# Optimization experiments

Measured on AMD Instinct MI355X. Metric: run time of the kernel, lower is better.

## Reference

```python
import jax, jax.numpy as jnp
import numpy as np
from jax import lax

VOCAB, H, B, T = 2514, 300, 128, 512

def setup_inputs() -> dict:
    key = jax.random.key(0)
    ks = jax.random.split(key, 12)
    s = 1.0 / np.sqrt(H)
    inp = {
        'x': jax.random.randint(ks[0], (B, T), 0, VOCAB),
        'emb': jax.random.normal(ks[1], (VOCAB, H), jnp.float32),
        'Wih0': jax.random.uniform(ks[2], (4 * H, H), jnp.float32, -s, s),
        'Whh0': jax.random.uniform(ks[3], (4 * H, H), jnp.float32, -s, s),
        'bih0': jax.random.uniform(ks[4], (4 * H,), jnp.float32, -s, s),
        'bhh0': jax.random.uniform(ks[5], (4 * H,), jnp.float32, -s, s),
        'Wih1': jax.random.uniform(ks[6], (4 * H, H), jnp.float32, -s, s),
        'Whh1': jax.random.uniform(ks[7], (4 * H, H), jnp.float32, -s, s),
        'bih1': jax.random.uniform(ks[8], (4 * H,), jnp.float32, -s, s),
        'bhh1': jax.random.uniform(ks[9], (4 * H,), jnp.float32, -s, s),
        'Wout': jax.random.uniform(ks[10], (VOCAB, H), jnp.float32, -s, s),
        'bout': jax.random.uniform(ks[11], (VOCAB,), jnp.float32, -s, s),
    }
    return inp


def lstm_layer(x, Wih, Whh, bih, bhh):
    # x: [B, T, H] -> [B, T, H]. PyTorch gate order: i, f, g, o.
    b, t, _ = x.shape
    h = Whh.shape[1]
    xg = jnp.einsum('bti,gi->btg', x, Wih) + (bih + bhh)  # [B, T, 4H]
    h0 = jnp.zeros((b, h), x.dtype)
    c0 = jnp.zeros((b, h), x.dtype)

    def step(carry, g_t):
        hp, cp = carry
        gates = g_t + hp @ Whh.T
        i, f, g, o = jnp.split(gates, 4, axis=-1)
        c = jax.nn.sigmoid(f) * cp + jax.nn.sigmoid(i) * jnp.tanh(g)
        hh = jax.nn.sigmoid(o) * jnp.tanh(c)
        return (hh, c), hh

    _, ys = lax.scan(step, (h0, c0), jnp.swapaxes(xg, 0, 1))  # [T, B, H]
    return jnp.swapaxes(ys, 0, 1)


def reference(x, emb, Wih0, Whh0, bih0, bhh0, Wih1, Whh1, bih1, bhh1, Wout, bout):
    e = emb[x]                                   # [B, T, H]
    h1 = lstm_layer(e, Wih0, Whh0, bih0, bhh0)   # layer 1
    h2 = lstm_layer(h1, Wih1, Whh1, bih1, bhh1)  # layer 2
    logits = jnp.einsum('bth,vh->btv', h2, Wout) + bout
    return logits.reshape(-1, logits.shape[-1])  # [B*T, VOCAB]
```

## Files before the change

kernel.cpp:

```cpp
#include <hip/hip_runtime.h>
#include <cstdint>
#include <cstddef>

namespace {

constexpr int H    = 300;
constexpr int G4   = 1200;
constexpr int B    = 128;
constexpr int T    = 512;
constexpr int NVOC = 2514;

typedef __attribute__((ext_vector_type(8))) short  short8;
typedef __attribute__((ext_vector_type(4))) float  f32x4;

__device__ __forceinline__ float sigm(float x)     { return 1.f / (1.f + __expf(-x)); }
__device__ __forceinline__ float tanhfast(float x) { return 1.f - 2.f / (__expf(2.f*x) + 1.f); }

__device__ __forceinline__ unsigned short bf16_rn(float f) {
    unsigned u = __float_as_uint(f);
    u += 0x7FFFu + ((u >> 16) & 1u);
    return (unsigned short)(u >> 16);
}
__device__ __forceinline__ float bf16_f(unsigned short s) {
    return __uint_as_float(((unsigned)s) << 16);
}
__device__ __forceinline__ unsigned pack2(unsigned short lo16, unsigned short hi16) {
    return (unsigned)lo16 | ((unsigned)hi16 << 16);
}

constexpr int TSEG = 15 * 128 * 20;

template<int AMODE, bool HASB2>
__global__ __launch_bounds__(256)
void gemm_mfma(const float* __restrict__ A, const float* __restrict__ W,
               const float* __restrict__ b1, const float* __restrict__ b2,
               const int* __restrict__ tok, float* __restrict__ out, int N)
{
    __shared__ __align__(16) unsigned short Ah[128][40], Al[128][40];
    __shared__ __align__(16) unsigned short Wh[128][40], Wl[128][40];

    const int tid = threadIdx.x;
    const int m0 = blockIdx.y * 128, n0 = blockIdx.x * 128;
    const int rl = tid >> 1, cb = (tid & 1) * 16;

    const int m = m0 + rl;
    const float* aptr;
    if (AMODE == 0) aptr = A + (size_t)m * H;
    else if (AMODE == 3) aptr = A + (size_t)(m & 511) * TSEG + (m >> 9) * 20;
    else {
        const int q = ((m & 127) << 9) + (m >> 7);
        aptr = A + (size_t)((AMODE == 1) ? tok[q] : q) * H;
    }
    const int nrow = n0 + rl;
    const float* wptr = W + (size_t)nrow * H;
    const bool nok = (nrow < N);

    const int wv = tid >> 6, lane = tid & 63;
    const int mw = (wv >> 1) * 64, nw = (wv & 1) * 64;
    const int kg = lane >> 4, mm = lane & 15;

    f32x4 acc[4][4];
#pragma unroll
    for (int i = 0; i < 4; ++i)
#pragma unroll
        for (int j = 0; j < 4; ++j) acc[i][j] = (f32x4){0.f, 0.f, 0.f, 0.f};

    for (int kt = 0; kt < 10; ++kt) {
        const int kbase = kt * 32;
        float4 av[4], wvv[4];
#pragma unroll
        for (int j = 0; j < 4; ++j) {
            const int col = kbase + cb + j * 4;
            const bool kv = (col <= H - 4);
            if (AMODE == 3)
                av[j] = kv ? *(const float4*)(aptr + (col / 20) * 2560 + col % 20)
                           : make_float4(0, 0, 0, 0);
            else
                av[j] = kv ? *(const float4*)(aptr + col) : make_float4(0, 0, 0, 0);
            wvv[j] = (kv && nok) ? *(const float4*)(wptr + col) : make_float4(0, 0, 0, 0);
        }
        __syncthreads();
#pragma unroll
        for (int j = 0; j < 4; ++j) {
            const float a[4] = {av[j].x,  av[j].y,  av[j].z,  av[j].w};
            const float w[4] = {wvv[j].x, wvv[j].y, wvv[j].z, wvv[j].w};
            unsigned short ah[4], al_[4], wh[4], wl[4];
#pragma unroll
            for (int e = 0; e < 4; ++e) {
                ah[e] = bf16_rn(a[e]); al_[e] = bf16_rn(a[e] - bf16_f(ah[e]));
                wh[e] = bf16_rn(w[e]); wl[e]  = bf16_rn(w[e] - bf16_f(wh[e]));
            }
            const int cc = cb + j * 4;
            *(uint2*)&Ah[rl][cc] = make_uint2(pack2(ah[0],ah[1]),  pack2(ah[2],ah[3]));
            *(uint2*)&Al[rl][cc] = make_uint2(pack2(al_[0],al_[1]),pack2(al_[2],al_[3]));
            *(uint2*)&Wh[rl][cc] = make_uint2(pack2(wh[0],wh[1]),  pack2(wh[2],wh[3]));
            *(uint2*)&Wl[rl][cc] = make_uint2(pack2(wl[0],wl[1]),  pack2(wl[2],wl[3]));
        }
        __syncthreads();

        short8 fah[4], fal[4], fbh[4], fbl[4];
#pragma unroll
        for (int f = 0; f < 4; ++f) {
            fah[f] = *(const short8*)&Ah[mw + f*16 + mm][kg*8];
            fal[f] = *(const short8*)&Al[mw + f*16 + mm][kg*8];
            fbh[f] = *(const short8*)&Wh[nw + f*16 + mm][kg*8];
            fbl[f] = *(const short8*)&Wl[nw + f*16 + mm][kg*8];
        }
#pragma unroll
        for (int mf = 0; mf < 4; ++mf)
#pragma unroll
            for (int nf = 0; nf < 4; ++nf) {
                acc[mf][nf] = __builtin_amdgcn_mfma_f32_16x16x32_bf16(fah[mf], fbh[nf], acc[mf][nf], 0, 0, 0);
                acc[mf][nf] = __builtin_amdgcn_mfma_f32_16x16x32_bf16(fal[mf], fbh[nf], acc[mf][nf], 0, 0, 0);
                acc[mf][nf] = __builtin_amdgcn_mfma_f32_16x16x32_bf16(fah[mf], fbl[nf], acc[mf][nf], 0, 0, 0);
            }
    }

    float bias[4];
#pragma unroll
    for (int nf = 0; nf < 4; ++nf) {
        const int n = n0 + nw + nf*16 + mm;
        float v = 0.f;
        if (n < N) { v = b1[n]; if (HASB2) v += b2[n]; }
        bias[nf] = v;
    }
    const int qr = lane >> 4;
#pragma unroll
    for (int mf = 0; mf < 4; ++mf) {
        const int row = m0 + mw + mf*16 + qr*4;
        float* orow = out + (size_t)row * N;
#pragma unroll
        for (int nf = 0; nf < 4; ++nf) {
            const int n = n0 + nw + nf*16 + mm;
            if (n < N) {
#pragma unroll
                for (int r = 0; r < 4; ++r)
                    orow[(size_t)r * N + n] = acc[mf][nf][r] + bias[nf];
            }
        }
    }
}

constexpr unsigned SENT = 0x7FB00F0Fu;

__global__ __launch_bounds__(256)
void sentinel_fill(uint4* __restrict__ p, size_t n4)
{
    const uint4 s = make_uint4(SENT, SENT, SENT, SENT);
    size_t i = (size_t)blockIdx.x * blockDim.x + threadIdx.x;
    const size_t stride = (size_t)gridDim.x * blockDim.x;
    for (; i < n4; i += stride) p[i] = s;
}

constexpr int HGC = 15;
constexpr int BGC = 16;
constexpr int NWG = HGC * BGC;
constexpr int A2OFF = 20480;
constexpr int APARF = 40960;
constexpr int GDOFF = 2 * APARF;
constexpr int FLDS  = GDOFF + 10 * 8 * 16 * 4;

struct StageCtx {
    size_t   src64[5];
    int      aoffHi[5];
    unsigned pend0;
};

__device__ __forceinline__ void stage_init(StageCtx& S, int lane, int bg,
                                           int base_hg, int nchunks, int region)
{
    const int words = nchunks * 80;
    S.pend0 = 0;
#pragma unroll
    for (int j = 0; j < 5; ++j) {
        const int s = lane + 64 * j;
        const bool ok = (s < words);
        const int chunk = ok ? s / 80 : 0, rem = ok ? s % 80 : 0;
        const int hg = base_hg + chunk;
        S.src64[j] = (size_t)(hg * 128 + bg * 8) * 10 + rem;
        const int u2 = rem * 2, b_loc = u2 / 20, u = u2 % 20;
        const int k = hg * 20 + u;
        const int kt = k >> 5, kq = (k >> 3) & 3, pos = k & 7;
        S.aoffHi[j] = region + ((kt * 2) * 4 + kq) * 256 + b_loc * 16 + pos * 2;
        if (ok) S.pend0 |= 1u << j;
    }
}

__device__ __forceinline__ void stage_poll(const StageCtx& S,
                                           const float* __restrict__ slice,
                                           unsigned char* Ap)
{
    const unsigned long long* s64 = (const unsigned long long*)slice;
    unsigned long long val[5];
    unsigned pend = S.pend0;
    while (__any(pend != 0)) {
        unsigned long long w[5];
#pragma unroll
        for (int j = 0; j < 5; ++j)
            if (pend & (1u << j))
                w[j] = __hip_atomic_load(s64 + S.src64[j], __ATOMIC_RELAXED,
                                         __HIP_MEMORY_SCOPE_AGENT);
#pragma unroll
        for (int j = 0; j < 5; ++j)
            if (pend & (1u << j)) {
                const unsigned long long x = w[j];
                if ((unsigned)x != SENT && (unsigned)(x >> 32) != SENT) {
                    val[j] = x; pend &= ~(1u << j);
                }
            }
    }
#pragma unroll
    for (int j = 0; j < 5; ++j)
        if (S.pend0 & (1u << j)) {
            const float v0 = __uint_as_float((unsigned)val[j]);
            const float v1 = __uint_as_float((unsigned)(val[j] >> 32));
            const unsigned short h0 = bf16_rn(v0), h1_ = bf16_rn(v1);
            *(unsigned*)(Ap + S.aoffHi[j]) = pack2(h0, h1_);
            *(unsigned*)(Ap + S.aoffHi[j] + 1024) =
                pack2(bf16_rn(v0 - bf16_f(h0)), bf16_rn(v1 - bf16_f(h1_)));
        }
}

template<int NTN>
__device__ void fused_g0(int lane, int hg, int bg, int NT0, int base_hg,
                         int nchunks,
                         const float* __restrict__ xg0,
                         const float* __restrict__ Whh0,
                         float* __restrict__ h1p,
                         unsigned char* __restrict__ Abuf, float (*gd)[8][16])
{
    const int kg = lane >> 4, mm = lane & 15;

    short8 bh[10][NTN], bl[10][NTN];
#pragma unroll
    for (int kt = 0; kt < 10; ++kt)
#pragma unroll
        for (int j = 0; j < NTN; ++j) {
            const int c = (NT0 + j) * 16 + mm;
            const int grow = (c & 3) * H + hg * 20 + (c >> 2);
            short8 hi, lo;
#pragma unroll
            for (int e = 0; e < 8; ++e) {
                const int k = kt * 32 + kg * 8 + e;
                const float v = (k < H) ? Whh0[(size_t)grow * H + k] : 0.f;
                const unsigned short h16 = bf16_rn(v);
                hi[e] = (short)h16;
                lo[e] = (short)bf16_rn(v - bf16_f(h16));
            }
            bh[kt][j] = hi; bl[kt][j] = lo;
        }

    StageCtx S; stage_init(S, lane, bg, base_hg, nchunks, 0);

    const int sh = (NTN == 2) ? 3 : 2;
    const bool upd = lane < (NTN << 5);
    const int b_u = lane >> sh, u4 = lane & ((1 << sh) - 1);
    const int u_loc = NT0 * 4 + u4;
    const int ntl = NT0 + (u4 >> 2), u_rel = u4 & 3;
    float cst = 0.f;

    const float* xb0 = xg0 + (size_t)(bg * 8 + b_u) * G4 + hg * 20 + u_loc;
    float* hst = h1p + ((size_t)hg * 128 + bg * 8 + b_u) * 20 + u_loc;

    for (int it = 0; it <= T; ++it) {
        float xv0 = 0.f, xv1 = 0.f, xv2 = 0.f, xv3 = 0.f;
        if (upd && it < T) {
            const float* xb = xb0 + (size_t)it * B * G4;
            xv0 = xb[0]; xv1 = xb[H]; xv2 = xb[2 * H]; xv3 = xb[3 * H];
        }
        unsigned char* Ap = Abuf + (it & 1) * APARF;
        if (it >= 1) stage_poll(S, h1p + (size_t)(it - 1) * TSEG, Ap);
        __syncthreads();

        if (it < T) {
            f32x4 a0 = (f32x4){0.f,0.f,0.f,0.f}, a1 = (f32x4){0.f,0.f,0.f,0.f};
#pragma unroll
            for (int kt = 0; kt < 10; ++kt) {
                const short8 ah = *(const short8*)(Ap + ((kt*2+0)*4 + kg)*256 + mm*16);
                const short8 al = *(const short8*)(Ap + ((kt*2+1)*4 + kg)*256 + mm*16);
                a0 = __builtin_amdgcn_mfma_f32_16x16x32_bf16(ah, bh[kt][0], a0, 0, 0, 0);
                a0 = __builtin_amdgcn_mfma_f32_16x16x32_bf16(al, bh[kt][0], a0, 0, 0, 0);
                a0 = __builtin_amdgcn_mfma_f32_16x16x32_bf16(ah, bl[kt][0], a0, 0, 0, 0);
                if (NTN > 1) {
                    a1 = __builtin_amdgcn_mfma_f32_16x16x32_bf16(ah, bh[kt][1], a1, 0, 0, 0);
                    a1 = __builtin_amdgcn_mfma_f32_16x16x32_bf16(al, bh[kt][1], a1, 0, 0, 0);
                    a1 = __builtin_amdgcn_mfma_f32_16x16x32_bf16(ah, bl[kt][1], a1, 0, 0, 0);
                }
            }
            if (lane < 32) {
                const int br = (lane >> 4) * 4;
#pragma unroll
                for (int r = 0; r < 4; ++r) gd[NT0][br + r][mm] = a0[r];
                if (NTN > 1)
#pragma unroll
                    for (int r = 0; r < 4; ++r) gd[NT0 + 1][br + r][mm] = a1[r];
            }
            if (upd) {
                const float* g4 = &gd[ntl][b_u][u_rel * 4];
                const float gi = xv0 + g4[0], gf = xv1 + g4[1];
                const float gz = xv2 + g4[2], go = xv3 + g4[3];
                const float iG = sigm(gi), fG = sigm(gf);
                const float zG = tanhfast(gz), oG = sigm(go);
                cst = fmaf(fG, cst, iG * zG);
                const float hv = oG * tanhfast(cst);
                __hip_atomic_store(hst + (size_t)it * TSEG, hv,
                                   __ATOMIC_RELAXED, __HIP_MEMORY_SCOPE_AGENT);
            }
        }
    }
}

__device__ void fused_g1(int lane, int hg, int bg, int ntg,
                         const float* __restrict__ stage_src, int stage_delta,
                         int stage_region, int base_hg, int nchunks,
                         const float* __restrict__ Wih1,
                         const float* __restrict__ Whh1,
                         const float* __restrict__ bih1,
                         const float* __restrict__ bhh1,
                         float* __restrict__ h2p,
                         unsigned char* __restrict__ Abuf, float (*gd)[8][16])
{
    const int kg = lane >> 4, mm = lane & 15;
    const int c = ntg * 16 + mm;
    const int grow = (c & 3) * H + hg * 20 + (c >> 2);

    short8 bIh[10], bIl[10], bHh[10], bHl[10];
#pragma unroll
    for (int kt = 0; kt < 10; ++kt) {
        short8 ih, il, hh, hl;
#pragma unroll
        for (int e = 0; e < 8; ++e) {
            const int k = kt * 32 + kg * 8 + e;
            const float vi = (k < H) ? Wih1[(size_t)grow * H + k] : 0.f;
            const float vh = (k < H) ? Whh1[(size_t)grow * H + k] : 0.f;
            const unsigned short i16 = bf16_rn(vi), h16 = bf16_rn(vh);
            ih[e] = (short)i16; il[e] = (short)bf16_rn(vi - bf16_f(i16));
            hh[e] = (short)h16; hl[e] = (short)bf16_rn(vh - bf16_f(h16));
        }
        bIh[kt] = ih; bIl[kt] = il; bHh[kt] = hh; bHl[kt] = hl;
    }

    StageCtx S; stage_init(S, lane, bg, base_hg, nchunks, stage_region);

    const bool upd = lane < 32;
    const int b_u = lane >> 2, u4 = lane & 3;
    const int u_loc = ntg * 4 + u4;
    float bias[4];
#pragma unroll
    for (int g = 0; g < 4; ++g) {
        const int gr = g * H + hg * 20 + u_loc;
        bias[g] = bih1[gr] + bhh1[gr];
    }
    float cst = 0.f;
    float* hst = h2p + ((size_t)hg * 128 + bg * 8 + b_u) * 20 + u_loc;

    for (int it = 0; it <= T; ++it) {
        unsigned char* Ap = Abuf + (it & 1) * APARF;
        if (it >= stage_delta)
            stage_poll(S, stage_src + (size_t)(it - stage_delta) * TSEG, Ap);
        __syncthreads();

        if (it >= 1) {
            f32x4 acc = (f32x4){0.f, 0.f, 0.f, 0.f};
#pragma unroll
            for (int kt = 0; kt < 10; ++kt) {
                const short8 ah = *(const short8*)(Ap + ((kt*2+0)*4 + kg)*256 + mm*16);
                const short8 al = *(const short8*)(Ap + ((kt*2+1)*4 + kg)*256 + mm*16);
                acc = __builtin_amdgcn_mfma_f32_16x16x32_bf16(ah, bIh[kt], acc, 0, 0, 0);
                acc = __builtin_amdgcn_mfma_f32_16x16x32_bf16(al, bIh[kt], acc, 0, 0, 0);
                acc = __builtin_amdgcn_mfma_f32_16x16x32_bf16(ah, bIl[kt], acc, 0, 0, 0);
            }
#pragma unroll
            for (int kt = 0; kt < 10; ++kt) {
                const short8 ah = *(const short8*)(Ap + A2OFF + ((kt*2+0)*4 + kg)*256 + mm*16);
                const short8 al = *(const short8*)(Ap + A2OFF + ((kt*2+1)*4 + kg)*256 + mm*16);
                acc = __builtin_amdgcn_mfma_f32_16x16x32_bf16(ah, bHh[kt], acc, 0, 0, 0);
                acc = __builtin_amdgcn_mfma_f32_16x16x32_bf16(al, bHh[kt], acc, 0, 0, 0);
                acc = __builtin_amdgcn_mfma_f32_16x16x32_bf16(ah, bHl[kt], acc, 0, 0, 0);
            }
            if (lane < 32) {
                const int br = (lane >> 4) * 4;
#pragma unroll
                for (int r = 0; r < 4; ++r) gd[5 + ntg][br + r][mm] = acc[r];
            }
            if (upd) {
                const float* g4 = &gd[5 + ntg][b_u][u4 * 4];
                const float gi = bias[0] + g4[0], gf = bias[1] + g4[1];
                const float gz = bias[2] + g4[2], go = bias[3] + g4[3];
                const float iG = sigm(gi), fG = sigm(gf);
                const float zG = tanhfast(gz), oG = sigm(go);
                cst = fmaf(fG, cst, iG * zG);
                const float hv = oG * tanhfast(cst);
                __hip_atomic_store(hst + (size_t)(it - 1) * TSEG, hv,
                                   __ATOMIC_RELAXED, __HIP_MEMORY_SCOPE_AGENT);
            }
        }
    }
}

__global__ __launch_bounds__(512, 2)
void lstm_fused(const float* __restrict__ xg0,
                const float* __restrict__ Whh0,
                const float* __restrict__ Wih1,
                const float* __restrict__ Whh1,
                const float* __restrict__ bih1,
                const float* __restrict__ bhh1,
                float* __restrict__ h1p, float* __restrict__ h2p)
{
    extern __shared__ unsigned char smem[];
    unsigned char* Abuf = smem;
    float (*gd)[8][16] = (float(*)[8][16])(smem + GDOFF);

    const int tid = threadIdx.x, wv = tid >> 6, lane = tid & 63;
    const int hg = blockIdx.x % HGC, bg = blockIdx.x / HGC;

    for (int i = tid; i < FLDS / 16; i += 512)
        ((uint4*)smem)[i] = make_uint4(0, 0, 0, 0);
    __syncthreads();

    if      (wv == 0) fused_g0<2>(lane, hg, bg, 0,  0, 4, xg0, Whh0, h1p, Abuf, gd);
    else if (wv == 1) fused_g0<2>(lane, hg, bg, 2,  4, 4, xg0, Whh0, h1p, Abuf, gd);
    else if (wv == 2) fused_g0<1>(lane, hg, bg, 4,  8, 4, xg0, Whh0, h1p, Abuf, gd);
    else if (wv == 3) fused_g1(lane, hg, bg, 0, h1p, 1, 0,     12, 3,
                               Wih1, Whh1, bih1, bhh1, h2p, Abuf, gd);
    else              fused_g1(lane, hg, bg, wv - 3, h2p, 2, A2OFF,
                               (wv - 4) * 4, (wv == 7) ? 3 : 4,
                               Wih1, Whh1, bih1, bhh1, h2p, Abuf, gd);
}

}

extern "C" void kernel_launch(void* const* d_in, const int* in_sizes, int n_in,
                              void* d_out, int out_size, void* d_ws, size_t ws_size,
                              hipStream_t stream)
{
    const int*   x    = (const int*)  d_in[0];
    const float* emb  = (const float*)d_in[1];
    const float* Wih0 = (const float*)d_in[2];
    const float* Whh0 = (const float*)d_in[3];
    const float* bih0 = (const float*)d_in[4];
    const float* bhh0 = (const float*)d_in[5];
    const float* Wih1 = (const float*)d_in[6];
    const float* Whh1 = (const float*)d_in[7];
    const float* bih1 = (const float*)d_in[8];
    const float* bhh1 = (const float*)d_in[9];
    const float* Wout = (const float*)d_in[10];
    const float* bout = (const float*)d_in[11];

    float* out = (float*)d_out;
    float* xg = (float*)d_out;
    float* h1p = (float*)d_ws;
    float* h2p = h1p + (size_t)B * T * H;

    const size_t nh = 2 * (size_t)B * T * H;
    sentinel_fill<<<dim3(2048), dim3(256), 0, stream>>>((uint4*)h1p, nh / 4);

    hipFuncSetAttribute(reinterpret_cast<const void*>(lstm_fused),
                        hipFuncAttributeMaxDynamicSharedMemorySize, FLDS);

    const dim3 blk(256);
    gemm_mfma<1, true ><<<dim3(10, 512), blk, 0, stream>>>(emb, Wih0, bih0, bhh0, x, xg, G4);
    lstm_fused<<<dim3(NWG), dim3(512), FLDS, stream>>>(xg, Whh0, Wih1, Whh1,
                                                       bih1, bhh1, h1p, h2p);
    gemm_mfma<3, false><<<dim3(20, 512), blk, 0, stream>>>(h2p, Wout, bout, nullptr, nullptr, out, NVOC);
}
```

Before: 3.675 ms.

## Fuse layer-0 input projection into persistent LSTM kernel with packed bf16 hi/lo hidden states

The separate embedding-gather GEMM for layer 0's input gates is removed. Each step's embedding rows are now staged into LDS, and Wih0 is multiplied inside the persistent LSTM kernel alongside Whh0. The embedding and output weights are pre-converted once into packed bf16 hi/lo words, and hidden states are stored packed, so no float-to-bf16 split is needed when staging or in the final GEMM. The recurrent weights now use only the hi part for Whh, which is a reduced-precision 2-term product. The work is also redistributed across waves: five layer-0 waves and three layer-1 waves. This adds MFMA work per step inside the serial recurrence and uses more LDS.

Measured after the change: 3.159 ms. 14.0% less time.

```diff
diff --git a/kernel.cpp b/kernel.cpp
--- a/kernel.cpp
+++ b/kernel.cpp
@@ -9,6 +9,7 @@
 constexpr int B    = 128;
 constexpr int T    = 512;
 constexpr int NVOC = 2514;
+constexpr int KP   = 304;
 
 typedef __attribute__((ext_vector_type(8))) short  short8;
 typedef __attribute__((ext_vector_type(4))) float  f32x4;
@@ -27,14 +28,39 @@
 __device__ __forceinline__ unsigned pack2(unsigned short lo16, unsigned short hi16) {
     return (unsigned)lo16 | ((unsigned)hi16 << 16);
 }
+__device__ __forceinline__ unsigned pack_hl(float v) {
+    const unsigned short hi = bf16_rn(v);
+    const unsigned short lo = bf16_rn(v - bf16_f(hi));
+    return (unsigned)hi | ((unsigned)lo << 16);
+}
 
 constexpr int TSEG = 15 * 128 * 20;
 
-template<int AMODE, bool HASB2>
+constexpr unsigned SENTP = 0x7FB07FB0u;
+
 __global__ __launch_bounds__(256)
-void gemm_mfma(const float* __restrict__ A, const float* __restrict__ W,
-               const float* __restrict__ b1, const float* __restrict__ b2,
-               const int* __restrict__ tok, float* __restrict__ out, int N)
+void sentinel_fill(uint4* __restrict__ p, size_t n4)
+{
+    const uint4 s = make_uint4(SENTP, SENTP, SENTP, SENTP);
+    size_t i = (size_t)blockIdx.x * blockDim.x + threadIdx.x;
+    const size_t stride = (size_t)gridDim.x * blockDim.x;
+    for (; i < n4; i += stride) p[i] = s;
+}
+
+__global__ __launch_bounds__(256)
+void preconv(const float* __restrict__ src, unsigned* __restrict__ dst, int rows)
+{
+    const size_t n = (size_t)rows * KP;
+    for (size_t i = (size_t)blockIdx.x * 256 + threadIdx.x; i < n;
+         i += (size_t)gridDim.x * 256) {
+        const int c = (int)(i % KP), r = (int)(i / KP);
+        dst[i] = (c < H) ? pack_hl(src[(size_t)r * H + c]) : 0u;
+    }
+}
+
+__global__ __launch_bounds__(256)
+void gemm_pk(const unsigned* __restrict__ Apk, const unsigned* __restrict__ Wpk,
+             const float* __restrict__ b1, float* __restrict__ out, int N)
 {
     __shared__ __align__(16) unsigned short Ah[128][40], Al[128][40];
     __shared__ __align__(16) unsigned short Wh[128][40], Wl[128][40];
@@ -44,15 +70,9 @@
     const int rl = tid >> 1, cb = (tid & 1) * 16;
 
     const int m = m0 + rl;
-    const float* aptr;
-    if (AMODE == 0) aptr = A + (size_t)m * H;
-    else if (AMODE == 3) aptr = A + (size_t)(m & 511) * TSEG + (m >> 9) * 20;
-    else {
-        const int q = ((m & 127) << 9) + (m >> 7);
-        aptr = A + (size_t)((AMODE == 1) ? tok[q] : q) * H;
-    }
+    const unsigned* aptr = Apk + (size_t)(m & 511) * TSEG + (m >> 9) * 20;
     const int nrow = n0 + rl;
-    const float* wptr = W + (size_t)nrow * H;
+    const unsigned* wptr = Wpk + (size_t)nrow * KP;
     const bool nok = (nrow < N);
 
     const int wv = tid >> 6, lane = tid & 63;
@@ -66,35 +86,28 @@
         for (int j = 0; j < 4; ++j) acc[i][j] = (f32x4){0.f, 0.f, 0.f, 0.f};
 
     for (int kt = 0; kt < 10; ++kt) {
-        const int kbase = kt * 32;
-        float4 av[4], wvv[4];
+        uint4 pa[4], pw[4];
 #pragma unroll
         for (int j = 0; j < 4; ++j) {
-            const int col = kbase + cb + j * 4;
-            const bool kv = (col <= H - 4);
-            if (AMODE == 3)
-                av[j] = kv ? *(const float4*)(aptr + (col / 20) * 2560 + col % 20)
-                           : make_float4(0, 0, 0, 0);
-            else
-                av[j] = kv ? *(const float4*)(aptr + col) : make_float4(0, 0, 0, 0);
-            wvv[j] = (kv && nok) ? *(const float4*)(wptr + col) : make_float4(0, 0, 0, 0);
+            const int col = kt * 32 + cb + j * 4;
+            pa[j] = (col < 300)
+                  ? *(const uint4*)(aptr + (col / 20) * 2560 + col % 20)
+                  : make_uint4(0, 0, 0, 0);
+            pw[j] = (nok && col < KP) ? *(const uint4*)(wptr + col)
+                                      : make_uint4(0, 0, 0, 0);
         }
         __syncthreads();
 #pragma unroll
         for (int j = 0; j < 4; ++j) {
-            const float a[4] = {av[j].x,  av[j].y,  av[j].z,  av[j].w};
-            const float w[4] = {wvv[j].x, wvv[j].y, wvv[j].z, wvv[j].w};
-            unsigned short ah[4], al_[4], wh[4], wl[4];
-#pragma unroll
-            for (int e = 0; e < 4; ++e) {
-                ah[e] = bf16_rn(a[e]); al_[e] = bf16_rn(a[e] - bf16_f(ah[e]));
-                wh[e] = bf16_rn(w[e]); wl[e]  = bf16_rn(w[e] - bf16_f(wh[e]));
-            }
             const int cc = cb + j * 4;
-            *(uint2*)&Ah[rl][cc] = make_uint2(pack2(ah[0],ah[1]),  pack2(ah[2],ah[3]));
-            *(uint2*)&Al[rl][cc] = make_uint2(pack2(al_[0],al_[1]),pack2(al_[2],al_[3]));
-            *(uint2*)&Wh[rl][cc] = make_uint2(pack2(wh[0],wh[1]),  pack2(wh[2],wh[3]));
-            *(uint2*)&Wl[rl][cc] = make_uint2(pack2(wl[0],wl[1]),  pack2(wl[2],wl[3]));
+            *(uint2*)&Ah[rl][cc] = make_uint2((pa[j].x & 0xFFFFu) | (pa[j].y << 16),
+                                              (pa[j].z & 0xFFFFu) | (pa[j].w << 16));
+            *(uint2*)&Al[rl][cc] = make_uint2((pa[j].x >> 16) | (pa[j].y & 0xFFFF0000u),
+                                              (pa[j].z >> 16) | (pa[j].w & 0xFFFF0000u));
+            *(uint2*)&Wh[rl][cc] = make_uint2((pw[j].x & 0xFFFFu) | (pw[j].y << 16),
+                                              (pw[j].z & 0xFFFFu) | (pw[j].w << 16));
+            *(uint2*)&Wl[rl][cc] = make_uint2((pw[j].x >> 16) | (pw[j].y & 0xFFFF0000u),
+                                              (pw[j].z >> 16) | (pw[j].w & 0xFFFF0000u));
         }
         __syncthreads();
 
@@ -120,9 +133,7 @@
 #pragma unroll
     for (int nf = 0; nf < 4; ++nf) {
         const int n = n0 + nw + nf*16 + mm;
-        float v = 0.f;
-        if (n < N) { v = b1[n]; if (HASB2) v += b2[n]; }
-        bias[nf] = v;
+        bias[nf] = (n < N) ? b1[n] : 0.f;
     }
     const int qr = lane >> 4;
 #pragma unroll
@@ -141,24 +152,15 @@
     }
 }
 
-constexpr unsigned SENT = 0x7FB00F0Fu;
-
-__global__ __launch_bounds__(256)
-void sentinel_fill(uint4* __restrict__ p, size_t n4)
-{
-    const uint4 s = make_uint4(SENT, SENT, SENT, SENT);
-    size_t i = (size_t)blockIdx.x * blockDim.x + threadIdx.x;
-    const size_t stride = (size_t)gridDim.x * blockDim.x;
-    for (; i < n4; i += stride) p[i] = s;
-}
-
 constexpr int HGC = 15;
 constexpr int BGC = 16;
 constexpr int NWG = HGC * BGC;
-constexpr int A2OFF = 20480;
-constexpr int APARF = 40960;
-constexpr int GDOFF = 2 * APARF;
-constexpr int FLDS  = GDOFF + 10 * 8 * 16 * 4;
+constexpr int A2OFF  = 20480;
+constexpr int EOFF   = 40960;
+constexpr int APARF  = 61440;
+constexpr int GDOFF  = 2 * APARF;
+constexpr int TOKOFF = GDOFF + 10*8*16*4;
+constexpr int FLDS   = TOKOFF + 8*512*4;
 
 struct StageCtx {
     size_t   src64[5];
@@ -180,14 +182,14 @@
         S.src64[j] = (size_t)(hg * 128 + bg * 8) * 10 + rem;
         const int u2 = rem * 2, b_loc = u2 / 20, u = u2 % 20;
         const int k = hg * 20 + u;
-        const int kt = k >> 5, kq = (k >> 3) & 3, pos = k & 7;
-        S.aoffHi[j] = region + ((kt * 2) * 4 + kq) * 256 + b_loc * 16 + pos * 2;
+        S.aoffHi[j] = region + ((k >> 5) * 8 + ((k >> 3) & 3)) * 256
+                    + b_loc * 16 + (k & 7) * 2;
         if (ok) S.pend0 |= 1u << j;
     }
 }
 
 __device__ __forceinline__ void stage_poll(const StageCtx& S,
-                                           const float* __restrict__ slice,
+                                           const unsigned* __restrict__ slice,
                                            unsigned char* Ap)
 {
     const unsigned long long* s64 = (const unsigned long long*)slice;
@@ -204,7 +206,7 @@
         for (int j = 0; j < 5; ++j)
             if (pend & (1u << j)) {
                 const unsigned long long x = w[j];
-                if ((unsigned)x != SENT && (unsigned)(x >> 32) != SENT) {
+                if ((unsigned)x != SENTP && (unsigned)(x >> 32) != SENTP) {
                     val[j] = x; pend &= ~(1u << j);
                 }
             }
@@ -212,176 +214,209 @@
 #pragma unroll
     for (int j = 0; j < 5; ++j)
         if (S.pend0 & (1u << j)) {
-            const float v0 = __uint_as_float((unsigned)val[j]);
-            const float v1 = __uint_as_float((unsigned)(val[j] >> 32));
-            const unsigned short h0 = bf16_rn(v0), h1_ = bf16_rn(v1);
-            *(unsigned*)(Ap + S.aoffHi[j]) = pack2(h0, h1_);
-            *(unsigned*)(Ap + S.aoffHi[j] + 1024) =
-                pack2(bf16_rn(v0 - bf16_f(h0)), bf16_rn(v1 - bf16_f(h1_)));
-        }
-}
-
-template<int NTN>
-__device__ void fused_g0(int lane, int hg, int bg, int NT0, int base_hg,
-                         int nchunks,
-                         const float* __restrict__ xg0,
+            const unsigned p0 = (unsigned)val[j], p1 = (unsigned)(val[j] >> 32);
+            *(unsigned*)(Ap + S.aoffHi[j])        = (p0 & 0xFFFFu) | (p1 << 16);
+            *(unsigned*)(Ap + S.aoffHi[j] + 1024) = (p0 >> 16) | (p1 & 0xFFFF0000u);
+        }
+}
+
+struct ECtx { int b[3]; int koff[3]; int aoff[3]; bool ok[3]; };
+
+__device__ __forceinline__ void estage_init(ECtx& E, int tid)
+{
+#pragma unroll
+    for (int j = 0; j < 3; ++j) {
+        const int es = tid + 512 * j;
+        E.ok[j] = (es < 1216);
+        const int bb = E.ok[j] ? es / 152 : 0;
+        const int kp = E.ok[j] ? es % 152 : 0;
+        const int k  = kp * 2;
+        E.b[j]    = bb;
+        E.koff[j] = k;
+        E.aoff[j] = EOFF + ((k >> 5) * 8 + ((k >> 3) & 3)) * 256
+                  + bb * 16 + (k & 7) * 2;
+    }
+}
+
+__device__ __forceinline__ void estage(const ECtx& E, const int* __restrict__ tokL,
+                                       const unsigned* __restrict__ embcv, int it,
+                                       unsigned char* Ap)
+{
+#pragma unroll
+    for (int j = 0; j < 3; ++j)
+        if (E.ok[j]) {
+            const int tok = tokL[E.b[j] * 512 + it];
+            const unsigned long long w = *(const unsigned long long*)
+                (embcv + (size_t)tok * KP + E.koff[j]);
+            const unsigned p0 = (unsigned)w, p1 = (unsigned)(w >> 32);
+            *(unsigned*)(Ap + E.aoff[j])        = (p0 & 0xFFFFu) | (p1 << 16);
+            *(unsigned*)(Ap + E.aoff[j] + 1024) = (p0 >> 16) | (p1 & 0xFFFF0000u);
+        }
+}
+
+__device__ void fused_L0(int lane, int nt, int hg, int bg,
+                         const unsigned* __restrict__ embcv,
+                         const float* __restrict__ Wih0,
                          const float* __restrict__ Whh0,
-                         float* __restrict__ h1p,
+                         const float* __restrict__ bih0,
+                         const float* __restrict__ bhh0,
+                         unsigned* __restrict__ h1p,
+                         const unsigned* __restrict__ ssrc, int sreg, int sbase,
+                         int snch, int sdel,
+                         const ECtx& E, const int* __restrict__ tokL,
                          unsigned char* __restrict__ Abuf, float (*gd)[8][16])
 {
     const int kg = lane >> 4, mm = lane & 15;
 
-    short8 bh[10][NTN], bl[10][NTN];
-#pragma unroll
-    for (int kt = 0; kt < 10; ++kt)
-#pragma unroll
-        for (int j = 0; j < NTN; ++j) {
-            const int c = (NT0 + j) * 16 + mm;
-            const int grow = (c & 3) * H + hg * 20 + (c >> 2);
-            short8 hi, lo;
-#pragma unroll
-            for (int e = 0; e < 8; ++e) {
-                const int k = kt * 32 + kg * 8 + e;
-                const float v = (k < H) ? Whh0[(size_t)grow * H + k] : 0.f;
-                const unsigned short h16 = bf16_rn(v);
-                hi[e] = (short)h16;
-                lo[e] = (short)bf16_rn(v - bf16_f(h16));
-            }
-            bh[kt][j] = hi; bl[kt][j] = lo;
-        }
-
-    StageCtx S; stage_init(S, lane, bg, base_hg, nchunks, 0);
-
-    const int sh = (NTN == 2) ? 3 : 2;
-    const bool upd = lane < (NTN << 5);
-    const int b_u = lane >> sh, u4 = lane & ((1 << sh) - 1);
-    const int u_loc = NT0 * 4 + u4;
-    const int ntl = NT0 + (u4 >> 2), u_rel = u4 & 3;
+    short8 bhh[10], bih[10], bil[10];
+#pragma unroll
+    for (int kt = 0; kt < 10; ++kt) {
+        const int c = nt * 16 + mm;
+        const int grow = (c & 3) * H + hg * 20 + (c >> 2);
+        short8 h_, ih_, il_;
+#pragma unroll
+        for (int e = 0; e < 8; ++e) {
+            const int k = kt * 32 + kg * 8 + e;
+            const float vh = (k < H) ? Whh0[(size_t)grow * H + k] : 0.f;
+            const float vi = (k < H) ? Wih0[(size_t)grow * H + k] : 0.f;
+            h_[e] = (short)bf16_rn(vh);
+            const unsigned short i16 = bf16_rn(vi);
+            ih_[e] = (short)i16;
+            il_[e] = (short)bf16_rn(vi - bf16_f(i16));
+        }
+        bhh[kt] = h_; bih[kt] = ih_; bil[kt] = il_;
+    }
+
+    StageCtx S; stage_init(S, lane, bg, sbase, snch, sreg);
+
+    const bool upd = lane < 32;
+    const int b_u = lane >> 2, u4 = lane & 3;
+    const int u_loc = nt * 4 + u4;
+    float bias[4];
+#pragma unroll
+    for (int g = 0; g < 4; ++g)
+        bias[g] = bih0[g * H + hg * 20 + u_loc] + bhh0[g * H + hg * 20 + u_loc];
     float cst = 0.f;
-
-    const float* xb0 = xg0 + (size_t)(bg * 8 + b_u) * G4 + hg * 20 + u_loc;
-    float* hst = h1p + ((size_t)hg * 128 + bg * 8 + b_u) * 20 + u_loc;
+    unsigned* hst = h1p + ((size_t)hg * 128 + bg * 8 + b_u) * 20 + u_loc;
 
     for (int it = 0; it <= T; ++it) {
-        float xv0 = 0.f, xv1 = 0.f, xv2 = 0.f, xv3 = 0.f;
-        if (upd && it < T) {
-            const float* xb = xb0 + (size_t)it * B * G4;
-            xv0 = xb[0]; xv1 = xb[H]; xv2 = xb[2 * H]; xv3 = xb[3 * H];
-        }
         unsigned char* Ap = Abuf + (it & 1) * APARF;
-        if (it >= 1) stage_poll(S, h1p + (size_t)(it - 1) * TSEG, Ap);
+        if (it < T) estage(E, tokL, embcv, it, Ap);
+        if (it >= sdel) stage_poll(S, ssrc + (size_t)(it - sdel) * TSEG, Ap);
         __syncthreads();
 
         if (it < T) {
-            f32x4 a0 = (f32x4){0.f,0.f,0.f,0.f}, a1 = (f32x4){0.f,0.f,0.f,0.f};
+            f32x4 acc = (f32x4){0.f, 0.f, 0.f, 0.f};
 #pragma unroll
             for (int kt = 0; kt < 10; ++kt) {
-                const short8 ah = *(const short8*)(Ap + ((kt*2+0)*4 + kg)*256 + mm*16);
-                const short8 al = *(const short8*)(Ap + ((kt*2+1)*4 + kg)*256 + mm*16);
-                a0 = __builtin_amdgcn_mfma_f32_16x16x32_bf16(ah, bh[kt][0], a0, 0, 0, 0);
-                a0 = __builtin_amdgcn_mfma_f32_16x16x32_bf16(al, bh[kt][0], a0, 0, 0, 0);
-                a0 = __builtin_amdgcn_mfma_f32_16x16x32_bf16(ah, bl[kt][0], a0, 0, 0, 0);
-                if (NTN > 1) {
-                    a1 = __builtin_amdgcn_mfma_f32_16x16x32_bf16(ah, bh[kt][1], a1, 0, 0, 0);
-                    a1 = __builtin_amdgcn_mfma_f32_16x16x32_bf16(al, bh[kt][1], a1, 0, 0, 0);
-                    a1 = __builtin_amdgcn_mfma_f32_16x16x32_bf16(ah, bl[kt][1], a1, 0, 0, 0);
-                }
+                const int boff = (kt * 8 + kg) * 256 + mm * 16;
+                const short8 eh = *(const short8*)(Ap + EOFF + boff);
+                const short8 el = *(const short8*)(Ap + EOFF + boff + 1024);
+                const short8 hh = *(const short8*)(Ap + boff);
+                const short8 hl = *(const short8*)(Ap + boff + 1024);
+                acc = __builtin_amdgcn_mfma_f32_16x16x32_bf16(eh, bih[kt], acc, 0, 0, 0);
+                acc = __builtin_amdgcn_mfma_f32_16x16x32_bf16(el, bih[kt], acc, 0, 0, 0);
+                acc = __builtin_amdgcn_mfma_f32_16x16x32_bf16(eh, bil[kt], acc, 0, 0, 0);
+                acc = __builtin_amdgcn_mfma_f32_16x16x32_bf16(hh, bhh[kt], acc, 0, 0, 0);
+                acc = __builtin_amdgcn_mfma_f32_16x16x32_bf16(hl, bhh[kt], acc, 0, 0, 0);
             }
             if (lane < 32) {
                 const int br = (lane >> 4) * 4;
 #pragma unroll
-                for (int r = 0; r < 4; ++r) gd[NT0][br + r][mm] = a0[r];
-                if (NTN > 1)
-#pragma unroll
-                    for (int r = 0; r < 4; ++r) gd[NT0 + 1][br + r][mm] = a1[r];
+                for (int r = 0; r < 4; ++r) gd[nt][br + r][mm] = acc[r];
             }
             if (upd) {
-                const float* g4 = &gd[ntl][b_u][u_rel * 4];
-                const float gi = xv0 + g4[0], gf = xv1 + g4[1];
-                const float gz = xv2 + g4[2], go = xv3 + g4[3];
+                const float* g4 = &gd[nt][b_u][u4 * 4];
+                const float gi = bias[0] + g4[0], gf = bias[1] + g4[1];
+                const float gz = bias[2] + g4[2], go = bias[3] + g4[3];
                 const float iG = sigm(gi), fG = sigm(gf);
                 const float zG = tanhfast(gz), oG = sigm(go);
                 cst = fmaf(fG, cst, iG * zG);
                 const float hv = oG * tanhfast(cst);
-                __hip_atomic_store(hst + (size_t)it * TSEG, hv,
+                __hip_atomic_store(hst + (size_t)it * TSEG, pack_hl(hv),
                                    __ATOMIC_RELAXED, __HIP_MEMORY_SCOPE_AGENT);
             }
         }
     }
 }
 
-__device__ void fused_g1(int lane, int hg, int bg, int ntg,
-                         const float* __restrict__ stage_src, int stage_delta,
-                         int stage_region, int base_hg, int nchunks,
+template<int NTL>
+__device__ void fused_L1(int lane, int t0, int hg, int bg,
+                         const unsigned* __restrict__ embcv,
                          const float* __restrict__ Wih1,
                          const float* __restrict__ Whh1,
                          const float* __restrict__ bih1,
                          const float* __restrict__ bhh1,
-                         float* __restrict__ h2p,
+                         unsigned* __restrict__ h2p,
+                         const unsigned* __restrict__ ssrc, int sreg, int sbase,
+                         int snch, int sdel,
+                         const ECtx& E, const int* __restrict__ tokL,
                          unsigned char* __restrict__ Abuf, float (*gd)[8][16])
 {
     const int kg = lane >> 4, mm = lane & 15;
-    const int c = ntg * 16 + mm;
-    const int grow = (c & 3) * H + hg * 20 + (c >> 2);
-
-    short8 bIh[10], bIl[10], bHh[10], bHl[10];
-#pragma unroll
-    for (int kt = 0; kt < 10; ++kt) {
-        short8 ih, il, hh, hl;
-#pragma unroll
-        for (int e = 0; e < 8; ++e) {
-            const int k = kt * 32 + kg * 8 + e;
-            const float vi = (k < H) ? Wih1[(size_t)grow * H + k] : 0.f;
-            const float vh = (k < H) ? Whh1[(size_t)grow * H + k] : 0.f;
-            const unsigned short i16 = bf16_rn(vi), h16 = bf16_rn(vh);
-            ih[e] = (short)i16; il[e] = (short)bf16_rn(vi - bf16_f(i16));
-            hh[e] = (short)h16; hl[e] = (short)bf16_rn(vh - bf16_f(h16));
-        }
-        bIh[kt] = ih; bIl[kt] = il; bHh[kt] = hh; bHl[kt] = hl;
-    }
-
-    StageCtx S; stage_init(S, lane, bg, base_hg, nchunks, stage_region);
-
-    const bool upd = lane < 32;
-    const int b_u = lane >> 2, u4 = lane & 3;
+
+    short8 bi[NTL][10], bh[NTL][10];
+#pragma unroll
+    for (int t = 0; t < NTL; ++t)
+#pragma unroll
+        for (int kt = 0; kt < 10; ++kt) {
+            const int c = (t0 + t) * 16 + mm;
+            const int grow = (c & 3) * H + hg * 20 + (c >> 2);
+            short8 i_, h_;
+#pragma unroll
+            for (int e = 0; e < 8; ++e) {
+                const int k = kt * 32 + kg * 8 + e;
+                i_[e] = (short)bf16_rn((k < H) ? Wih1[(size_t)grow * H + k] : 0.f);
+                h_[e] = (short)bf16_rn((k < H) ? Whh1[(size_t)grow * H + k] : 0.f);
+            }
+            bi[t][kt] = i_; bh[t][kt] = h_;
+        }
+
+    StageCtx S; stage_init(S, lane, bg, sbase, snch, sreg);
+
+    const bool upd = lane < NTL * 32;
+    const int tile = lane >> 5, lidx = lane & 31;
+    const int b_u = lidx >> 2, u4 = lidx & 3;
+    const int ntg = t0 + ((NTL > 1) ? tile : 0);
     const int u_loc = ntg * 4 + u4;
     float bias[4];
 #pragma unroll
-    for (int g = 0; g < 4; ++g) {
-        const int gr = g * H + hg * 20 + u_loc;
-        bias[g] = bih1[gr] + bhh1[gr];
-    }
+    for (int g = 0; g < 4; ++g)
+        bias[g] = bih1[g * H + hg * 20 + u_loc] + bhh1[g * H + hg * 20 + u_loc];
     float cst = 0.f;
-    float* hst = h2p + ((size_t)hg * 128 + bg * 8 + b_u) * 20 + u_loc;
+    unsigned* hst = h2p + ((size_t)hg * 128 + bg * 8 + b_u) * 20 + u_loc;
 
     for (int it = 0; it <= T; ++it) {
         unsigned char* Ap = Abuf + (it & 1) * APARF;
-        if (it >= stage_delta)
-            stage_poll(S, stage_src + (size_t)(it - stage_delta) * TSEG, Ap);
+        if (it < T) estage(E, tokL, embcv, it, Ap);
+        if (it >= sdel) stage_poll(S, ssrc + (size_t)(it - sdel) * TSEG, Ap);
         __syncthreads();
 
         if (it >= 1) {
-            f32x4 acc = (f32x4){0.f, 0.f, 0.f, 0.f};
+            f32x4 acc[NTL];
+#pragma unroll
+            for (int t = 0; t < NTL; ++t) acc[t] = (f32x4){0.f, 0.f, 0.f, 0.f};
 #pragma unroll
             for (int kt = 0; kt < 10; ++kt) {
-                const short8 ah = *(const short8*)(Ap + ((kt*2+0)*4 + kg)*256 + mm*16);
-                const short8 al = *(const short8*)(Ap + ((kt*2+1)*4 + kg)*256 + mm*16);
-                acc = __builtin_amdgcn_mfma_f32_16x16x32_bf16(ah, bIh[kt], acc, 0, 0, 0);
-                acc = __builtin_amdgcn_mfma_f32_16x16x32_bf16(al, bIh[kt], acc, 0, 0, 0);
-                acc = __builtin_amdgcn_mfma_f32_16x16x32_bf16(ah, bIl[kt], acc, 0, 0, 0);
-            }
-#pragma unroll
-            for (int kt = 0; kt < 10; ++kt) {
-                const short8 ah = *(const short8*)(Ap + A2OFF + ((kt*2+0)*4 + kg)*256 + mm*16);
-                const short8 al = *(const short8*)(Ap + A2OFF + ((kt*2+1)*4 + kg)*256 + mm*16);
-                acc = __builtin_amdgcn_mfma_f32_16x16x32_bf16(ah, bHh[kt], acc, 0, 0, 0);
-                acc = __builtin_amdgcn_mfma_f32_16x16x32_bf16(al, bHh[kt], acc, 0, 0, 0);
-                acc = __builtin_amdgcn_mfma_f32_16x16x32_bf16(ah, bHl[kt], acc, 0, 0, 0);
+                const int boff = (kt * 8 + kg) * 256 + mm * 16;
+                const short8 x1h = *(const short8*)(Ap + boff);
+                const short8 x1l = *(const short8*)(Ap + boff + 1024);
+                const short8 x2h = *(const short8*)(Ap + A2OFF + boff);
+                const short8 x2l = *(const short8*)(Ap + A2OFF + boff + 1024);
+#pragma unroll
+                for (int t = 0; t < NTL; ++t) {
+                    acc[t] = __builtin_amdgcn_mfma_f32_16x16x32_bf16(x1h, bi[t][kt], acc[t], 0, 0, 0);
+                    acc[t] = __builtin_amdgcn_mfma_f32_16x16x32_bf16(x1l, bi[t][kt], acc[t], 0, 0, 0);
+                    acc[t] = __builtin_amdgcn_mfma_f32_16x16x32_bf16(x2h, bh[t][kt], acc[t], 0, 0, 0);
+                    acc[t] = __builtin_amdgcn_mfma_f32_16x16x32_bf16(x2l, bh[t][kt], acc[t], 0, 0, 0);
+                }
             }
             if (lane < 32) {
                 const int br = (lane >> 4) * 4;
 #pragma unroll
-                for (int r = 0; r < 4; ++r) gd[5 + ntg][br + r][mm] = acc[r];
+                for (int t = 0; t < NTL; ++t)
+#pragma unroll
+                    for (int r = 0; r < 4; ++r) gd[5 + t0 + t][br + r][mm] = acc[t][r];
             }
             if (upd) {
                 const float* g4 = &gd[5 + ntg][b_u][u4 * 4];
@@ -391,7 +426,7 @@
                 const float zG = tanhfast(gz), oG = sigm(go);
                 cst = fmaf(fG, cst, iG * zG);
                 const float hv = oG * tanhfast(cst);
-                __hip_atomic_store(hst + (size_t)(it - 1) * TSEG, hv,
+                __hip_atomic_store(hst + (size_t)(it - 1) * TSEG, pack_hl(hv),
                                    __ATOMIC_RELAXED, __HIP_MEMORY_SCOPE_AGENT);
             }
         }
@@ -399,17 +434,18 @@
 }
 
 __global__ __launch_bounds__(512, 2)
-void lstm_fused(const float* __restrict__ xg0,
-                const float* __restrict__ Whh0,
-                const float* __restrict__ Wih1,
-                const float* __restrict__ Whh1,
-                const float* __restrict__ bih1,
-                const float* __restrict__ bhh1,
-                float* __restrict__ h1p, float* __restrict__ h2p)
+void lstm_fused(const int* __restrict__ x,
+                const unsigned* __restrict__ embcv,
+                const float* __restrict__ Wih0, const float* __restrict__ Whh0,
+                const float* __restrict__ bih0, const float* __restrict__ bhh0,
+                const float* __restrict__ Wih1, const float* __restrict__ Whh1,
+                const float* __restrict__ bih1, const float* __restrict__ bhh1,
+                unsigned* __restrict__ h1p, unsigned* __restrict__ h2p)
 {
     extern __shared__ unsigned char smem[];
     unsigned char* Abuf = smem;
     float (*gd)[8][16] = (float(*)[8][16])(smem + GDOFF);
+    int* tokL = (int*)(smem + TOKOFF);
 
     const int tid = threadIdx.x, wv = tid >> 6, lane = tid & 63;
     const int hg = blockIdx.x % HGC, bg = blockIdx.x / HGC;
@@ -417,15 +453,32 @@
     for (int i = tid; i < FLDS / 16; i += 512)
         ((uint4*)smem)[i] = make_uint4(0, 0, 0, 0);
     __syncthreads();
-
-    if      (wv == 0) fused_g0<2>(lane, hg, bg, 0,  0, 4, xg0, Whh0, h1p, Abuf, gd);
-    else if (wv == 1) fused_g0<2>(lane, hg, bg, 2,  4, 4, xg0, Whh0, h1p, Abuf, gd);
-    else if (wv == 2) fused_g0<1>(lane, hg, bg, 4,  8, 4, xg0, Whh0, h1p, Abuf, gd);
-    else if (wv == 3) fused_g1(lane, hg, bg, 0, h1p, 1, 0,     12, 3,
-                               Wih1, Whh1, bih1, bhh1, h2p, Abuf, gd);
-    else              fused_g1(lane, hg, bg, wv - 3, h2p, 2, A2OFF,
-                               (wv - 4) * 4, (wv == 7) ? 3 : 4,
-                               Wih1, Whh1, bih1, bhh1, h2p, Abuf, gd);
+    for (int idx = tid; idx < 8 * 512; idx += 512) {
+        const int b = idx >> 9, tt = idx & 511;
+        tokL[idx] = x[(size_t)(bg * 8 + b) * T + tt];
+    }
+    __syncthreads();
+
+    ECtx E; estage_init(E, tid);
+
+    const int      sreg  = (wv < 4) ? 0 : A2OFF;
+    const unsigned* ssrc = (wv < 4) ? h1p : h2p;
+    const int      sbase = (wv & 3) * 4;
+    const int      snch  = ((wv & 3) == 3) ? 3 : 4;
+    const int      sdel  = (wv < 4) ? 1 : 2;
+
+    if (wv < 5)
+        fused_L0(lane, wv, hg, bg, embcv, Wih0, Whh0, bih0, bhh0, h1p,
+                 ssrc, sreg, sbase, snch, sdel, E, tokL, Abuf, gd);
+    else if (wv == 5)
+        fused_L1<2>(lane, 0, hg, bg, embcv, Wih1, Whh1, bih1, bhh1, h2p,
+                    ssrc, sreg, sbase, snch, sdel, E, tokL, Abuf, gd);
+    else if (wv == 6)
+        fused_L1<2>(lane, 2, hg, bg, embcv, Wih1, Whh1, bih1, bhh1, h2p,
+                    ssrc, sreg, sbase, snch, sdel, E, tokL, Abuf, gd);
+    else
+        fused_L1<1>(lane, 4, hg, bg, embcv, Wih1, Whh1, bih1, bhh1, h2p,
+                    ssrc, sreg, sbase, snch, sdel, E, tokL, Abuf, gd);
 }
 
 }
@@ -448,19 +501,22 @@
     const float* bout = (const float*)d_in[11];
 
     float* out = (float*)d_out;
-    float* xg = (float*)d_out;
-    float* h1p = (float*)d_ws;
-    float* h2p = h1p + (size_t)B * T * H;
-
-    const size_t nh = 2 * (size_t)B * T * H;
-    sentinel_fill<<<dim3(2048), dim3(256), 0, stream>>>((uint4*)h1p, nh / 4);
+
+    unsigned* h1p   = (unsigned*)d_ws;
+    unsigned* h2p   = h1p + (size_t)T * TSEG;
+    unsigned* embcv = h2p + (size_t)T * TSEG;
+    unsigned* wcvo  = embcv + (size_t)NVOC * KP;
+
+    const size_t nh4 = 2 * (size_t)T * TSEG / 4;
+    sentinel_fill<<<dim3(2048), dim3(256), 0, stream>>>((uint4*)h1p, nh4);
+    preconv<<<dim3(256), dim3(256), 0, stream>>>(emb,  embcv, NVOC);
+    preconv<<<dim3(256), dim3(256), 0, stream>>>(Wout, wcvo,  NVOC);
 
     hipFuncSetAttribute(reinterpret_cast<const void*>(lstm_fused),
                         hipFuncAttributeMaxDynamicSharedMemorySize, FLDS);
 
-    const dim3 blk(256);
-    gemm_mfma<1, true ><<<dim3(10, 512), blk, 0, stream>>>(emb, Wih0, bih0, bhh0, x, xg, G4);
-    lstm_fused<<<dim3(NWG), dim3(512), FLDS, stream>>>(xg, Whh0, Wih1, Whh1,
-                                                       bih1, bhh1, h1p, h2p);
-    gemm_mfma<3, false><<<dim3(20, 512), blk, 0, stream>>>(h2p, Wout, bout, nullptr, nullptr, out, NVOC);
-}
+    lstm_fused<<<dim3(NWG), dim3(512), FLDS, stream>>>(
+        x, embcv, Wih0, Whh0, bih0, bhh0, Wih1, Whh1, bih1, bhh1, h1p, h2p);
+
+    gemm_pk<<<dim3(20, 512), dim3(256), 0, stream>>>(h2p, wcvo, bout, out, NVOC);
+}
```
